# Optimization experiments

Hardware: AMD Instinct MI355X
Metric: run time of the kernel (lower is better)

Reference implementation:

```python
import jax, jax.numpy as jnp
import numpy as np

B, N, M, D = 64, 16384, 64, 512
EPS = 1e-16


def setup_inputs() -> dict:
    key = jax.random.key(0)
    k1, k2, k3, k4 = jax.random.split(key, 4)
    controller_output = jax.random.normal(k1, (B, D), dtype=jnp.float32)
    w_prev = jax.random.uniform(k2, (B, N), dtype=jnp.float32)
    memory = jax.random.normal(k3, (B, N, M), dtype=jnp.float32)
    W = jax.random.normal(k4, (M + 6, D), dtype=jnp.float32) * (1.0 / np.sqrt(D))
    b = jnp.zeros((M + 6,), dtype=jnp.float32)
    return {"controller_output": controller_output, "w_prev": w_prev,
            "memory": memory, "W": W, "b": b}


def reference(controller_output, w_prev, memory, W, b):
    # fc_read projection -> [B, M+6], split into k, beta, g, s, gamma
    o = controller_output @ W.T + b
    k = o[:, :M]                      # [B, M] content key
    beta = jax.nn.softplus(o[:, M:M + 1])        # [B, 1] key strength
    g = jax.nn.sigmoid(o[:, M + 1:M + 2])        # [B, 1] interpolation gate
    s = jax.nn.softmax(o[:, M + 2:M + 5], axis=1)  # [B, 3] shift weights
    gamma = 1.0 + jax.nn.softplus(o[:, M + 5:M + 6])  # [B, 1] sharpening

    # content addressing: cosine similarity between k and each memory row
    num = jnp.einsum('bm,bnm->bn', k, memory)                      # [B, N]
    denom = (jnp.linalg.norm(k, axis=1, keepdims=True)
             * jnp.linalg.norm(memory, axis=2) + EPS)              # [B, N]
    w_c = jax.nn.softmax(beta * (num / denom), axis=1)             # [B, N]

    # interpolation with previous weighting
    w_g = g * w_c + (1.0 - g) * w_prev                              # [B, N]

    # circular convolution shift over {-1, 0, +1}
    w_t = (s[:, 0:1] * jnp.roll(w_g, 1, axis=1)
           + s[:, 1:2] * w_g
           + s[:, 2:3] * jnp.roll(w_g, -1, axis=1))                 # [B, N]

    # sharpening
    w_pow = w_t ** gamma
    w = w_pow / (jnp.sum(w_pow, axis=1, keepdims=True) + EPS)       # [B, N]

    # read: weighted sum of memory rows
    r = jnp.einsum('bn,bnm->bm', w, memory)                         # [B, M]
    return (r, w)
```

## Files before the change

### kernel.cpp

```cpp
#include <hip/hip_runtime.h>
#include <math.h>

#define B 64
#define N 16384
#define MDIM 64
#define DDIM 512
#define EPSF 1e-16f

#define K_OFF      0
#define SCAL_OFF   (B*64)
#define SCORE_OFF  (SCAL_OFF + B*8)
#define MS_OFF     (SCORE_OFF + B*N)
#define MXI_OFF    (MS_OFF + B*64)
#define PSUM_OFF   (MXI_OFF + B*2)
#define INVP_OFF   (PSUM_OFF + B*32)
#define PART_OFF   (INVP_OFF + B)

__device__ __forceinline__ float rowsum16(float x) {
    float t;
    t = __int_as_float(__builtin_amdgcn_update_dpp(0, __float_as_int(x), 0x128, 0xF, 0xF, true)); x += t;
    t = __int_as_float(__builtin_amdgcn_update_dpp(0, __float_as_int(x), 0x124, 0xF, 0xF, true)); x += t;
    t = __int_as_float(__builtin_amdgcn_update_dpp(0, __float_as_int(x), 0x122, 0xF, 0xF, true)); x += t;
    t = __int_as_float(__builtin_amdgcn_update_dpp(0, __float_as_int(x), 0x121, 0xF, 0xF, true)); x += t;
    return x;
}

__global__ __launch_bounds__(256) void k1(const float* __restrict__ c,
                                          const float* __restrict__ W,
                                          const float* __restrict__ bias,
                                          float* __restrict__ ws) {
    int b = blockIdx.x;
    __shared__ float cs[DDIM];
    __shared__ float osh[72];
    int tid = threadIdx.x;
    for (int i = tid; i < DDIM; i += 256) cs[i] = c[b * DDIM + i];
    __syncthreads();
    int wave = tid >> 6, lane = tid & 63;
    for (int j = wave; j < MDIM + 6; j += 4) {
        const float* wr = W + (size_t)j * DDIM;
        float sum = 0.f;
        for (int d = lane; d < DDIM; d += 64) sum += cs[d] * wr[d];
        for (int off = 32; off > 0; off >>= 1) sum += __shfl_xor(sum, off);
        if (lane == 0) osh[j] = sum + bias[j];
    }
    __syncthreads();
    if (tid < 64) ws[K_OFF + b * 64 + tid] = osh[tid];
    if (wave == 0) {
        float v = osh[lane];
        float sq = v * v;
        for (int off = 32; off > 0; off >>= 1) sq += __shfl_xor(sq, off);
        if (lane == 0) {
            float kn = sqrtf(sq);
            float ob = osh[64], og = osh[65], os0 = osh[66], os1 = osh[67],
                  os2 = osh[68], ogm = osh[69];
            float beta  = fmaxf(ob, 0.f) + log1pf(expf(-fabsf(ob)));
            float g     = 1.f / (1.f + expf(-og));
            float mx    = fmaxf(os0, fmaxf(os1, os2));
            float e0 = expf(os0 - mx), e1 = expf(os1 - mx), e2 = expf(os2 - mx);
            float es = e0 + e1 + e2;
            float gamma = 1.f + fmaxf(ogm, 0.f) + log1pf(expf(-fabsf(ogm)));
            float* sc = ws + SCAL_OFF + b * 8;
            sc[0] = kn; sc[1] = beta; sc[2] = g;
            sc[3] = e0 / es; sc[4] = e1 / es; sc[5] = e2 / es;
            sc[6] = gamma;
        }
    }
}

__global__ __launch_bounds__(256) void k2(const float* __restrict__ mem,
                                          float* __restrict__ ws) {
    int b = blockIdx.x >> 5, chunk = blockIdx.x & 31;
    __shared__ float ks[64];
    __shared__ float kb2[2];
    __shared__ float scbuf[512];
    int tid = threadIdx.x;
    if (tid < 64) ks[tid] = ws[K_OFF + b * 64 + tid];
    if (tid == 64) kb2[0] = ws[SCAL_OFF + b * 8 + 0];
    if (tid == 65) kb2[1] = ws[SCAL_OFF + b * 8 + 1];
    __syncthreads();
    float kn = kb2[0], beta = kb2[1];
    int grp = tid >> 4, ll = tid & 15;
    float k0 = ks[ll * 4], k1v = ks[ll * 4 + 1], k2v = ks[ll * 4 + 2], k3v = ks[ll * 4 + 3];
    int row0 = chunk * 512;
    #pragma unroll 8
    for (int it = 0; it < 32; ++it) {
        int lrow = it * 16 + grp;
        int row = row0 + lrow;
        float4 v = *reinterpret_cast<const float4*>(
            mem + ((size_t)b * N + row) * MDIM + ll * 4);
        float dot = v.x * k0 + v.y * k1v + v.z * k2v + v.w * k3v;
        float sq  = v.x * v.x + v.y * v.y + v.z * v.z + v.w * v.w;
        dot = rowsum16(dot);
        sq  = rowsum16(sq);
        if (ll == 0) {
            float score = beta * (dot / (kn * sqrtf(sq) + EPSF));
            ws[SCORE_OFF + (size_t)b * N + row] = score;
            scbuf[lrow] = score;
        }
    }
    __syncthreads();
    if (tid < 64) {
        float vr[8];
        float m = -1e30f;
        #pragma unroll
        for (int j = 0; j < 8; ++j) {
            vr[j] = scbuf[tid + 64 * j];
            m = fmaxf(m, vr[j]);
        }
        #pragma unroll
        for (int off = 32; off > 0; off >>= 1) m = fmaxf(m, __shfl_xor(m, off));
        float s = 0.f;
        #pragma unroll
        for (int j = 0; j < 8; ++j) s += __expf(vr[j] - m);
        #pragma unroll
        for (int off = 32; off > 0; off >>= 1) s += __shfl_xor(s, off);
        if (tid == 0) {
            ws[MS_OFF + ((size_t)b * 32 + chunk) * 2]     = m;
            ws[MS_OFF + ((size_t)b * 32 + chunk) * 2 + 1] = s;
        }
    }
}

__global__ __launch_bounds__(64) void kc(float* __restrict__ ws) {
    int b = blockIdx.x, lane = threadIdx.x;
    float m = -1e30f, s = 0.f;
    if (lane < 32) {
        m = ws[MS_OFF + ((size_t)b * 32 + lane) * 2];
        s = ws[MS_OFF + ((size_t)b * 32 + lane) * 2 + 1];
    }
    #pragma unroll
    for (int off = 32; off > 0; off >>= 1) {
        float m2 = __shfl_xor(m, off), s2 = __shfl_xor(s, off);
        float M = fmaxf(m, m2);
        s = s * __expf(m - M) + s2 * __expf(m2 - M);
        m = M;
    }
    if (lane == 0) {
        ws[MXI_OFF + b * 2]     = m;
        ws[MXI_OFF + b * 2 + 1] = 1.f / s;
    }
}

__global__ __launch_bounds__(256) void kwb(const float* __restrict__ w_prev,
                                           float* __restrict__ ws,
                                           float* __restrict__ w_out) {
    int b = blockIdx.x >> 5, chunk = blockIdx.x & 31;
    int tid = threadIdx.x, wave = tid >> 6, lane = tid & 63;
    __shared__ float wgL[514];
    __shared__ float red[4];
    const float* sl = ws + SCAL_OFF + b * 8;
    float g = sl[2], s0 = sl[3], s1 = sl[4], s2 = sl[5], gamma = sl[6];
    float mx  = ws[MXI_OFF + b * 2];
    float inv = ws[MXI_OFF + b * 2 + 1];
    const float* sc = ws + SCORE_OFF + (size_t)b * N;
    const float* wp = w_prev + (size_t)b * N;
    int row0 = chunk * 512;

    {
        int r0 = row0 + tid;
        wgL[tid + 1]   = g * (__expf(sc[r0] - mx) * inv) + (1.f - g) * wp[r0];
        int r1 = row0 + tid + 256;
        wgL[tid + 257] = g * (__expf(sc[r1] - mx) * inv) + (1.f - g) * wp[r1];
        if (tid == 0) {
            int rl = (row0 - 1) & (N - 1);
            wgL[0] = g * (__expf(sc[rl] - mx) * inv) + (1.f - g) * wp[rl];
        }
        if (tid == 255) {
            int rr = (row0 + 512) & (N - 1);
            wgL[513] = g * (__expf(sc[rr] - mx) * inv) + (1.f - g) * wp[rr];
        }
    }
    __syncthreads();

    float wt0 = s0 * wgL[tid]       + s1 * wgL[tid + 1]   + s2 * wgL[tid + 2];
    float wt1 = s0 * wgL[tid + 256] + s1 * wgL[tid + 257] + s2 * wgL[tid + 258];
    float p0 = __expf(gamma * __logf(wt0));
    float p1 = __expf(gamma * __logf(wt1));
    float* wo = w_out + (size_t)b * N + row0;
    wo[tid]       = p0;
    wo[tid + 256] = p1;

    float sp = p0 + p1;
    #pragma unroll
    for (int off = 32; off > 0; off >>= 1) sp += __shfl_xor(sp, off);
    if (lane == 0) red[wave] = sp;
    __syncthreads();
    if (tid == 0)
        ws[PSUM_OFF + b * 32 + chunk] = red[0] + red[1] + red[2] + red[3];
}

__global__ __launch_bounds__(64) void kpp(float* __restrict__ ws) {
    int b = blockIdx.x, lane = threadIdx.x;
    float s = (lane < 32) ? ws[PSUM_OFF + b * 32 + lane] : 0.f;
    #pragma unroll
    for (int off = 32; off > 0; off >>= 1) s += __shfl_xor(s, off);
    if (lane == 0) ws[INVP_OFF + b] = 1.f / (s + EPSF);
}

__global__ __launch_bounds__(256) void kr(const float* __restrict__ mem,
                                          float* __restrict__ w_out,
                                          const float* __restrict__ ws,
                                          float* __restrict__ part) {
    int b = blockIdx.x >> 5, chunk = blockIdx.x & 31;
    int tid = threadIdx.x, grp = tid >> 4, ll = tid & 15;
    float invp = ws[INVP_OFF + b];
    float* wpow = w_out + (size_t)b * N;
    float4 acc = make_float4(0.f, 0.f, 0.f, 0.f);
    int row0 = chunk * 512;
    #pragma unroll 8
    for (int it = 0; it < 32; ++it) {
        int row = row0 + it * 16 + grp;
        float wv = wpow[row];
        float4 v = *reinterpret_cast<const float4*>(
            mem + ((size_t)b * N + row) * MDIM + ll * 4);
        acc.x += wv * v.x; acc.y += wv * v.y; acc.z += wv * v.z; acc.w += wv * v.w;
    }
    __shared__ float lds[16][64];
    lds[grp][ll * 4 + 0] = acc.x * invp;
    lds[grp][ll * 4 + 1] = acc.y * invp;
    lds[grp][ll * 4 + 2] = acc.z * invp;
    lds[grp][ll * 4 + 3] = acc.w * invp;
    __syncthreads();
    {
        float a0 = wpow[row0 + tid] * invp;
        float a1 = wpow[row0 + tid + 256] * invp;
        wpow[row0 + tid]       = a0;
        wpow[row0 + tid + 256] = a1;
    }
    if (tid < 64) {
        float sacc = 0.f;
        #pragma unroll
        for (int gi = 0; gi < 16; ++gi) sacc += lds[gi][tid];
        part[(size_t)blockIdx.x * 64 + tid] = sacc;
    }
}

__global__ __launch_bounds__(64) void krr(const float* __restrict__ part,
                                          float* __restrict__ r) {
    int b = blockIdx.x, m = threadIdx.x;
    float s = 0.f;
    #pragma unroll
    for (int c = 0; c < 32; ++c) s += part[((size_t)b * 32 + c) * 64 + m];
    r[b * 64 + m] = s;
}

extern "C" void kernel_launch(void* const* d_in, const int* in_sizes, int n_in,
                              void* d_out, int out_size, void* d_ws, size_t ws_size,
                              hipStream_t stream) {
    const float* c      = (const float*)d_in[0];
    const float* w_prev = (const float*)d_in[1];
    const float* mem    = (const float*)d_in[2];
    const float* W      = (const float*)d_in[3];
    const float* bias   = (const float*)d_in[4];
    float* out = (float*)d_out;
    float* r_out = out;
    float* w_out = out + B * MDIM;
    float* ws = (float*)d_ws;

    k1 <<<B,      256, 0, stream>>>(c, W, bias, ws);
    k2 <<<B * 32, 256, 0, stream>>>(mem, ws);
    kc <<<B,       64, 0, stream>>>(ws);
    kwb<<<B * 32, 256, 0, stream>>>(w_prev, ws, w_out);
    kpp<<<B,       64, 0, stream>>>(ws);
    kr <<<B * 32, 256, 0, stream>>>(mem, w_out, ws, ws + PART_OFF);
    krr<<<B,       64, 0, stream>>>(ws + PART_OFF, r_out);
}
```

Measured before the change: 116.6 us.

## Fuse sharpened-weight computation with memory read and defer normalization

Merges the weight-building kernel and the memory-read kernel so each block computes its unnormalized sharpened weights into shared memory and immediately uses them to accumulate its partial read vector. Normalization by the total sum is deferred: the small reduction kernel computes the inverse sum, scales r, and a new light kernel rescales w. This removes one kernel launch and the global round-trip of w between kernels, at the cost of an extra pass over w for the final scaling.

```diff
diff --git a/kernel.cpp b/kernel.cpp
--- a/kernel.cpp
+++ b/kernel.cpp
@@ -141,12 +141,16 @@
     }
 }
 
-__global__ __launch_bounds__(256) void kwb(const float* __restrict__ w_prev,
+__global__ __launch_bounds__(256) void krw(const float* __restrict__ mem,
+                                           const float* __restrict__ w_prev,
                                            float* __restrict__ ws,
-                                           float* __restrict__ w_out) {
+                                           float* __restrict__ w_out,
+                                           float* __restrict__ part) {
     int b = blockIdx.x >> 5, chunk = blockIdx.x & 31;
     int tid = threadIdx.x, wave = tid >> 6, lane = tid & 63;
     __shared__ float wgL[514];
+    __shared__ float wpl[512];
+    __shared__ float lds[16][64];
     __shared__ float red[4];
     const float* sl = ws + SCAL_OFF + b * 8;
     float g = sl[2], s0 = sl[3], s1 = sl[4], s2 = sl[5], gamma = sl[6];
@@ -176,6 +180,8 @@
     float wt1 = s0 * wgL[tid + 256] + s1 * wgL[tid + 257] + s2 * wgL[tid + 258];
     float p0 = __expf(gamma * __logf(wt0));
     float p1 = __expf(gamma * __logf(wt1));
+    wpl[tid] = p0;
+    wpl[tid + 256] = p1;
     float* wo = w_out + (size_t)b * N + row0;
     wo[tid]       = p0;
     wo[tid + 256] = p1;
@@ -187,46 +193,22 @@
     __syncthreads();
     if (tid == 0)
         ws[PSUM_OFF + b * 32 + chunk] = red[0] + red[1] + red[2] + red[3];
-}
-
-__global__ __launch_bounds__(64) void kpp(float* __restrict__ ws) {
-    int b = blockIdx.x, lane = threadIdx.x;
-    float s = (lane < 32) ? ws[PSUM_OFF + b * 32 + lane] : 0.f;
-    #pragma unroll
-    for (int off = 32; off > 0; off >>= 1) s += __shfl_xor(s, off);
-    if (lane == 0) ws[INVP_OFF + b] = 1.f / (s + EPSF);
-}
-
-__global__ __launch_bounds__(256) void kr(const float* __restrict__ mem,
-                                          float* __restrict__ w_out,
-                                          const float* __restrict__ ws,
-                                          float* __restrict__ part) {
-    int b = blockIdx.x >> 5, chunk = blockIdx.x & 31;
-    int tid = threadIdx.x, grp = tid >> 4, ll = tid & 15;
-    float invp = ws[INVP_OFF + b];
-    float* wpow = w_out + (size_t)b * N;
+
+    int grp = tid >> 4, ll = tid & 15;
     float4 acc = make_float4(0.f, 0.f, 0.f, 0.f);
-    int row0 = chunk * 512;
     #pragma unroll 8
     for (int it = 0; it < 32; ++it) {
-        int row = row0 + it * 16 + grp;
-        float wv = wpow[row];
+        int lrow = it * 16 + grp;
+        float wv = wpl[lrow];
         float4 v = *reinterpret_cast<const float4*>(
-            mem + ((size_t)b * N + row) * MDIM + ll * 4);
+            mem + ((size_t)b * N + row0 + lrow) * MDIM + ll * 4);
         acc.x += wv * v.x; acc.y += wv * v.y; acc.z += wv * v.z; acc.w += wv * v.w;
     }
-    __shared__ float lds[16][64];
-    lds[grp][ll * 4 + 0] = acc.x * invp;
-    lds[grp][ll * 4 + 1] = acc.y * invp;
-    lds[grp][ll * 4 + 2] = acc.z * invp;
-    lds[grp][ll * 4 + 3] = acc.w * invp;
-    __syncthreads();
-    {
-        float a0 = wpow[row0 + tid] * invp;
-        float a1 = wpow[row0 + tid + 256] * invp;
-        wpow[row0 + tid]       = a0;
-        wpow[row0 + tid + 256] = a1;
-    }
+    lds[grp][ll * 4 + 0] = acc.x;
+    lds[grp][ll * 4 + 1] = acc.y;
+    lds[grp][ll * 4 + 2] = acc.z;
+    lds[grp][ll * 4 + 3] = acc.w;
+    __syncthreads();
     if (tid < 64) {
         float sacc = 0.f;
         #pragma unroll
@@ -236,12 +218,28 @@
 }
 
 __global__ __launch_bounds__(64) void krr(const float* __restrict__ part,
+                                          float* __restrict__ ws,
                                           float* __restrict__ r) {
-    int b = blockIdx.x, m = threadIdx.x;
-    float s = 0.f;
-    #pragma unroll
-    for (int c = 0; c < 32; ++c) s += part[((size_t)b * 32 + c) * 64 + m];
-    r[b * 64 + m] = s;
+    int b = blockIdx.x, tid = threadIdx.x;
+    float s = (tid < 32) ? ws[PSUM_OFF + b * 32 + tid] : 0.f;
+    #pragma unroll
+    for (int off = 32; off > 0; off >>= 1) s += __shfl_xor(s, off);
+    float invp = 1.f / (s + EPSF);
+    if (tid == 0) ws[INVP_OFF + b] = invp;
+    float srr = 0.f;
+    #pragma unroll
+    for (int c = 0; c < 32; ++c) srr += part[((size_t)b * 32 + c) * 64 + tid];
+    r[b * 64 + tid] = srr * invp;
+}
+
+__global__ __launch_bounds__(256) void kwf(const float* __restrict__ ws,
+                                           float* __restrict__ w_out) {
+    int b = blockIdx.x >> 5, chunk = blockIdx.x & 31;
+    int tid = threadIdx.x;
+    float invp = ws[INVP_OFF + b];
+    size_t base = (size_t)b * N + chunk * 512;
+    w_out[base + tid]       *= invp;
+    w_out[base + tid + 256] *= invp;
 }
 
 extern "C" void kernel_launch(void* const* d_in, const int* in_sizes, int n_in,
@@ -260,8 +258,7 @@
     k1 <<<B,      256, 0, stream>>>(c, W, bias, ws);
     k2 <<<B * 32, 256, 0, stream>>>(mem, ws);
     kc <<<B,       64, 0, stream>>>(ws);
-    kwb<<<B * 32, 256, 0, stream>>>(w_prev, ws, w_out);
-    kpp<<<B,       64, 0, stream>>>(ws);
-    kr <<<B * 32, 256, 0, stream>>>(mem, w_out, ws, ws + PART_OFF);
-    krr<<<B,       64, 0, stream>>>(ws + PART_OFF, r_out);
-}
+    krw<<<B * 32, 256, 0, stream>>>(mem, w_prev, ws, w_out, ws + PART_OFF);
+    krr<<<B,       64, 0, stream>>>(ws + PART_OFF, ws, r_out);
+    kwf<<<B * 32, 256, 0, stream>>>(ws, w_out);
+}
```

Measured after the change: 111.9 us. 4.1% less time.
